# Optimization experiments

Hardware: AMD Instinct MI355X
Metric: run time of the kernel (lower is better)

Reference implementation:

```python
import jax, jax.numpy as jnp
import numpy as np

N_NODES = 24576
N_EDGES = 294912
B_GRAPHS = 128
D_IN = 92
D = 512
H = 8
HD = D // H
L = 3
DFF = 4 * D
LN_EPS = 1e-5


def _layer_norm(x, g, b):
    mu = jnp.mean(x, axis=-1, keepdims=True)
    var = jnp.mean((x - mu) ** 2, axis=-1, keepdims=True)
    return (x - mu) * jax.lax.rsqrt(var + LN_EPS) * g + b


def setup_inputs() -> dict:
    key = jax.random.key(0)
    ks = jax.random.split(key, 24)
    s = 0.02
    inp = {
        "node_features": jax.random.normal(ks[0], (N_NODES, D_IN), jnp.float32),
        "edge_index": jax.random.randint(ks[1], (2, N_EDGES), 0, N_NODES, jnp.int64),
        "edge_attr": jax.random.uniform(ks[2], (N_EDGES,), jnp.float32),
        "batch": jnp.sort(jax.random.randint(ks[3], (N_NODES,), 0, B_GRAPHS, jnp.int64)),
        # atom embedding Linear(92 -> D)
        "emb_w": jax.random.normal(ks[4], (D, D_IN), jnp.float32) * s,
        "emb_b": jnp.zeros((D,), jnp.float32),
        # per-layer MHA params (stacked over L layers)
        "in_proj_w": jax.random.normal(ks[5], (L, 3 * D, D), jnp.float32) * s,
        "in_proj_b": jnp.zeros((L, 3 * D), jnp.float32),
        "out_w": jax.random.normal(ks[6], (L, D, D), jnp.float32) * s,
        "out_b": jnp.zeros((L, D), jnp.float32),
        "ln1_g": jnp.ones((L, D), jnp.float32),
        "ln1_b": jnp.zeros((L, D), jnp.float32),
        "ffn_w1": jax.random.normal(ks[7], (L, DFF, D), jnp.float32) * s,
        "ffn_b1": jnp.zeros((L, DFF), jnp.float32),
        "ffn_w2": jax.random.normal(ks[8], (L, D, DFF), jnp.float32) * s,
        "ffn_b2": jnp.zeros((L, D), jnp.float32),
        "ln2_g": jnp.ones((L, D), jnp.float32),
        "ln2_b": jnp.zeros((L, D), jnp.float32),
        # output head: Linear(D,D) -> SiLU -> Linear(D,1)
        "head_w1": jax.random.normal(ks[9], (D, D), jnp.float32) * s,
        "head_b1": jnp.zeros((D,), jnp.float32),
        "head_w2": jax.random.normal(ks[10], (1, D), jnp.float32) * s,
        "head_b2": jnp.zeros((1,), jnp.float32),
    }
    return inp


def _forward(node_features, batch, emb_w, emb_b, in_proj_w, in_proj_b, out_w,
             out_b, ln1_g, ln1_b, ffn_w1, ffn_b1, ffn_w2, ffn_b2, ln2_g,
             ln2_b, head_w1, head_b1, head_w2, head_b2):
    N = node_features.shape[0]
    B = int(jnp.max(batch)) + 1
    counts = jnp.bincount(batch, length=B)            # (B,) nodes per graph
    S = int(jnp.max(counts))                          # max_nodes
    starts = jnp.searchsorted(batch, jnp.arange(B))   # batch is sorted
    pos = jnp.arange(N) - starts[batch]               # slot within graph

    h = node_features @ emb_w.T + emb_b               # (N, D)
    # ragged -> dense pad  (B, S, D)
    hp = jnp.zeros((B, S, D), h.dtype).at[batch, pos].set(h)
    key_pad = jnp.arange(S)[None, :] >= counts[:, None]   # True = padding

    scale = 1.0 / jnp.sqrt(jnp.asarray(HD, hp.dtype))
    for l in range(L):
        qkv = hp @ in_proj_w[l].T + in_proj_b[l]      # (B, S, 3D)
        q, k, v = jnp.split(qkv, 3, axis=-1)
        q = q.reshape(B, S, H, HD).transpose(0, 2, 1, 3)
        k = k.reshape(B, S, H, HD).transpose(0, 2, 1, 3)
        v = v.reshape(B, S, H, HD).transpose(0, 2, 1, 3)
        scores = jnp.einsum('bhqd,bhkd->bhqk', q, k) * scale
        scores = jnp.where(key_pad[:, None, None, :], -jnp.inf, scores)
        attn = jax.nn.softmax(scores, axis=-1)
        o = jnp.einsum('bhqk,bhkd->bhqd', attn, v)
        o = o.transpose(0, 2, 1, 3).reshape(B, S, D)
        o = o @ out_w[l].T + out_b[l]
        x = _layer_norm(hp + o, ln1_g[l], ln1_b[l])   # post-norm
        f = jax.nn.relu(x @ ffn_w1[l].T + ffn_b1[l]) @ ffn_w2[l].T + ffn_b2[l]
        hp = _layer_norm(x + f, ln2_g[l], ln2_b[l])

    # unpad + segment mean pool
    h_out = hp[batch, pos]                            # (N, D)
    pooled = jax.ops.segment_sum(h_out, batch, num_segments=B)
    pooled = pooled / counts[:, None].astype(pooled.dtype)
    y = jax.nn.silu(pooled @ head_w1.T + head_b1) @ head_w2.T + head_b2
    return y                                          # (B, 1)


def reference(node_features, edge_index, edge_attr, batch, emb_w, emb_b,
              in_proj_w, in_proj_b, out_w, out_b, ln1_g, ln1_b, ffn_w1,
              ffn_b1, ffn_w2, ffn_b2, ln2_g, ln2_b, head_w1, head_b1,
              head_w2, head_b2):
    # edge_index / edge_attr are accepted but unused, matching the torch forward
    return _forward(node_features, batch, emb_w, emb_b, in_proj_w, in_proj_b,
                    out_w, out_b, ln1_g, ln1_b, ffn_w1, ffn_b1, ffn_w2,
                    ffn_b2, ln2_g, ln2_b, head_w1, head_b1, head_w2, head_b2)
```

## Files before the change

kernel.cpp:

```cpp
#include <hip/hip_runtime.h>
#include <hip/hip_bf16.h>
#include <cstdint>
#include <cfloat>
#include <cstddef>
#include <type_traits>

#define N_NODES 24576
#define B_GRAPHS 128
#define D_IN 92
#define D_INP 96
#define DMODEL 512
#define NHEAD 8
#define HDIM 64
#define NLAYER 3
#define DFF 2048

typedef __attribute__((ext_vector_type(8))) short short8;
typedef __attribute__((ext_vector_type(4))) short short4v;
typedef __attribute__((ext_vector_type(8))) unsigned short ushort8;
typedef __attribute__((ext_vector_type(4))) float f32x4;

__device__ __forceinline__ float b2f(unsigned short u) {
  union { unsigned int i; float f; } x;
  x.i = ((unsigned int)u) << 16;
  return x.f;
}
__device__ __forceinline__ unsigned short f2b(float f) {
  __hip_bfloat16 h = __float2bfloat16(f);
  return *reinterpret_cast<unsigned short*>(&h);
}

__device__ __forceinline__ void gl2lds16(const __hip_bfloat16* g,
                                         __hip_bfloat16* l) {
  __builtin_amdgcn_global_load_lds(
      (const __attribute__((address_space(1))) unsigned int*)g,
      (__attribute__((address_space(3))) unsigned int*)l, 16, 0, 0);
}

__global__ void starts_k(const int* __restrict__ batch32, int* __restrict__ starts) {
  __shared__ int is64_s;
  const int tid = threadIdx.x;
  if (tid == 0) is64_s = 0;
  __syncthreads();
  int bad = 0;
  for (int i = tid; i < N_NODES - 1; i += 256)
    if (batch32[i] > batch32[i + 1]) bad = 1;
  if (bad) atomicOr(&is64_s, 1);
  __syncthreads();
  const int is64 = is64_s;
  if (tid <= B_GRAPHS) {
    int lo = 0, hi = N_NODES;
    while (lo < hi) {
      int mid = (lo + hi) >> 1;
      int v = is64 ? batch32[2 * mid] : batch32[mid];
      if (v < tid) lo = mid + 1; else hi = mid;
    }
    starts[tid] = lo;
  }
}

__global__ __launch_bounds__(256) void cvt_k(const float* __restrict__ in,
                                             __hip_bfloat16* __restrict__ out,
                                             int count4) {
  int i = blockIdx.x * 256 + threadIdx.x;
  if (i < count4) {
    float4 v = ((const float4*)in)[i];
    short4v o;
    o[0] = (short)f2b(v.x); o[1] = (short)f2b(v.y);
    o[2] = (short)f2b(v.z); o[3] = (short)f2b(v.w);
    ((short4v*)out)[i] = o;
  }
}

__global__ __launch_bounds__(256) void padcvt_k(const float* __restrict__ in,
                                                __hip_bfloat16* __restrict__ out,
                                                int rows) {
  int idx = blockIdx.x * 256 + threadIdx.x;
  if (idx < rows * D_INP) {
    int r = idx / D_INP, c = idx - r * D_INP;
    out[idx] = __float2bfloat16(c < D_IN ? in[(size_t)r * D_IN + c] : 0.0f);
  }
}

__global__ __launch_bounds__(256) void mgemm_k(
    const __hip_bfloat16* __restrict__ A, const __hip_bfloat16* __restrict__ W,
    const float* __restrict__ bias, const __hip_bfloat16* __restrict__ res,
    __hip_bfloat16* __restrict__ C, int M, int N, int K, int act) {
  __shared__ __align__(16) __hip_bfloat16 As[2][128 * 32];
  __shared__ __align__(16) __hip_bfloat16 Ws[2][128 * 32];
  const int tid = threadIdx.x;
  const int wave = tid >> 6, lane = tid & 63;

  const int nxt = N >> 7, nmt = M >> 7;
  int rowt, colt;
  if ((nmt & 7) == 0) {
    const int rows_per = nmt >> 3;
    const int x = blockIdx.x & 7;
    const int j = blockIdx.x >> 3;
    rowt = x * rows_per + j % rows_per;
    colt = j / rows_per;
  } else {
    rowt = blockIdx.x / nxt;
    colt = blockIdx.x % nxt;
  }
  const int m0 = rowt * 128, n0 = colt * 128;

  const int mw = (wave >> 1) * 64, nw = (wave & 1) * 64;
  const int quad = lane >> 4, l16 = lane & 15;

  f32x4 acc[4][4] = {};

  const int srow = wave * 32 + (lane >> 2);
  const int skc = (lane & 3) * 8;
  const __hip_bfloat16* gA = A + (size_t)(m0 + srow) * K + skc;
  const __hip_bfloat16* gW = W + (size_t)(n0 + srow) * K + skc;
  const int lo = wave * 32 * 32;

  gl2lds16(gA, &As[0][lo]);
  gl2lds16(gA + (size_t)16 * K, &As[0][lo + 16 * 32]);
  gl2lds16(gW, &Ws[0][lo]);
  gl2lds16(gW + (size_t)16 * K, &Ws[0][lo + 16 * 32]);

  int cur = 0;
  for (int k0 = 0; k0 < K; k0 += 32) {
    __syncthreads();
    if (k0 + 32 < K) {
      const int nb = cur ^ 1;
      gl2lds16(gA + k0 + 32, &As[nb][lo]);
      gl2lds16(gA + (size_t)16 * K + k0 + 32, &As[nb][lo + 16 * 32]);
      gl2lds16(gW + k0 + 32, &Ws[nb][lo]);
      gl2lds16(gW + (size_t)16 * K + k0 + 32, &Ws[nb][lo + 16 * 32]);
    }
    short8 af[4], bf[4];
#pragma unroll
    for (int t = 0; t < 4; t++) {
      af[t] = *(const short8*)&As[cur][(mw + t * 16 + l16) * 32 + quad * 8];
      bf[t] = *(const short8*)&Ws[cur][(nw + t * 16 + l16) * 32 + quad * 8];
    }
#pragma unroll
    for (int mt = 0; mt < 4; mt++)
#pragma unroll
      for (int nt = 0; nt < 4; nt++)
        acc[mt][nt] = __builtin_amdgcn_mfma_f32_16x16x32_bf16(
            af[mt], bf[nt], acc[mt][nt], 0, 0, 0);
    cur ^= 1;
  }

#pragma unroll
  for (int mt = 0; mt < 4; mt++) {
#pragma unroll
    for (int nt = 0; nt < 4; nt++) {
      const int n = n0 + nw + nt * 16 + l16;
      const float bv = bias[n];
#pragma unroll
      for (int i = 0; i < 4; i++) {
        const int m = m0 + mw + mt * 16 + quad * 4 + i;
        float v = acc[mt][nt][i] + bv;
        if (res) v += __bfloat162float(res[(size_t)m * N + n]);
        if (act == 1) v = fmaxf(v, 0.0f);
        C[(size_t)m * N + n] = __float2bfloat16(v);
      }
    }
  }
}

__global__ __launch_bounds__(256) void gemm_k(
    const float* __restrict__ A, const float* __restrict__ W,
    const float* __restrict__ bias, const float* __restrict__ res,
    float* __restrict__ C, int M, int N, int K, int act) {
  __shared__ float As[16][68];
  __shared__ float Ws[16][68];
  const int tid = threadIdx.x;
  const int tx = tid & 15, ty = tid >> 4;
  const int m0 = blockIdx.y * 64, n0 = blockIdx.x * 64;
  const int lr = tid >> 2;
  const int lk = (tid & 3) * 4;
  float acc[4][4] = {{0.f}};
  for (int k0 = 0; k0 < K; k0 += 16) {
#pragma unroll
    for (int i = 0; i < 4; i++) {
      int k = k0 + lk + i;
      As[lk + i][lr] = (k < K) ? A[(size_t)(m0 + lr) * K + k] : 0.0f;
      Ws[lk + i][lr] = (k < K) ? W[(size_t)(n0 + lr) * K + k] : 0.0f;
    }
    __syncthreads();
#pragma unroll
    for (int kk = 0; kk < 16; kk++) {
      float4 a4 = *(const float4*)&As[kk][ty * 4];
      float4 w4 = *(const float4*)&Ws[kk][tx * 4];
      float a[4] = {a4.x, a4.y, a4.z, a4.w};
      float w[4] = {w4.x, w4.y, w4.z, w4.w};
#pragma unroll
      for (int i = 0; i < 4; i++)
#pragma unroll
        for (int j = 0; j < 4; j++) acc[i][j] += a[i] * w[j];
    }
    __syncthreads();
  }
#pragma unroll
  for (int i = 0; i < 4; i++) {
    int m = m0 + ty * 4 + i;
#pragma unroll
    for (int j = 0; j < 4; j++) {
      int n = n0 + tx * 4 + j;
      float v = acc[i][j] + bias[n];
      if (res) v += res[(size_t)m * N + n];
      if (act == 1) v = fmaxf(v, 0.0f);
      else if (act == 2) v = v / (1.0f + __expf(-v));
      C[(size_t)m * N + n] = v;
    }
  }
}

__global__ __launch_bounds__(256) void lnb_k(
    const __hip_bfloat16* __restrict__ in, const float* __restrict__ g,
    const float* __restrict__ b, __hip_bfloat16* __restrict__ out) {
  int row = blockIdx.x * 4 + (threadIdx.x >> 6);
  int lane = threadIdx.x & 63;
  const unsigned short* rp =
      (const unsigned short*)in + (size_t)row * DMODEL + lane * 8;
  ushort8 sv = *(const ushort8*)rp;
  float v[8];
  float s = 0.f;
#pragma unroll
  for (int i = 0; i < 8; i++) { v[i] = b2f(sv[i]); s += v[i]; }
#pragma unroll
  for (int off = 32; off; off >>= 1) s += __shfl_xor(s, off);
  float mu = s * (1.0f / DMODEL);
  float vs = 0.f;
#pragma unroll
  for (int i = 0; i < 8; i++) { float d = v[i] - mu; vs += d * d; }
#pragma unroll
  for (int off = 32; off; off >>= 1) vs += __shfl_xor(vs, off);
  float rs = rsqrtf(vs * (1.0f / DMODEL) + 1e-5f);
  ushort8 o;
#pragma unroll
  for (int i = 0; i < 8; i++) {
    int c = lane * 8 + i;
    o[i] = f2b((v[i] - mu) * rs * g[c] + b[c]);
  }
  *(ushort8*)((unsigned short*)out + (size_t)row * DMODEL + lane * 8) = o;
}

#define MAXNH 128
__global__ __launch_bounds__(256, 3) void attn5_k(
    const __hip_bfloat16* __restrict__ qkv, const int* __restrict__ starts,
    __hip_bfloat16* __restrict__ O1, __hip_bfloat16* __restrict__ O2,
    float* __restrict__ ml) {
  const int half = blockIdx.x & 1;
  const int gh = blockIdx.x >> 1;
  const int g = gh >> 3, h = gh & 7;
  int s0 = starts[g], s1 = starts[g + 1];
  s0 = min(max(s0, 0), N_NODES);
  s1 = min(max(s1, s0), N_NODES);
  const int n = s1 - s0, start = s0;
  if (n == 0) return;
  const int tid = threadIdx.x, wave = tid >> 6, lane = tid & 63;
  const int quad = lane >> 4, l16 = lane & 15;
  unsigned short* Oh = (unsigned short*)(half ? O2 : O1);

  __shared__ __align__(16) unsigned short Ks[128][72];
  __shared__ __align__(16) unsigned short Vt[64][136];
  __shared__ __align__(16) unsigned short Ps[4][16][136];

  if (n <= 2 * MAXNH) {
    const int nh1 = (n + 1) >> 1;
    const int k0g = half * nh1;
    const int nh = half ? (n - nh1) : nh1;
    const int ktq = (n + 15) >> 4;

    if (nh == 0) {
      for (int mt = wave; mt < ktq; mt += 4) {
        const int q = mt * 16 + l16;
        if (q < n) {
          short4v z = {0, 0, 0, 0};
#pragma unroll
          for (int dt = 0; dt < 4; dt++)
            *(short4v*)(Oh + (size_t)(start + q) * DMODEL + h * HDIM +
                        dt * 16 + quad * 4) = z;
          if (quad == 0) {
            float2 mlv = {-FLT_MAX, 0.0f};
            *(float2*)(ml + ((size_t)(start + q) * NHEAD + h) * 4 + half * 2) = mlv;
          }
        }
      }
      return;
    }

    for (int idx = tid; idx < nh * 8; idx += 256) {
      int r = idx >> 3, c = (idx & 7) * 8;
      *(ushort8*)&Ks[r][c] = *(const ushort8*)((const unsigned short*)qkv +
                                               (size_t)(start + k0g + r) * 1536 +
                                               512 + h * HDIM + c);
    }
    for (int idx = tid; idx < 16 * 8; idx += 256) {
      int r = nh + (idx >> 3), c = (idx & 7) * 8;
      if (r < 128) {
        ushort8 z = {0, 0, 0, 0, 0, 0, 0, 0};
        *(ushort8*)&Ks[r][c] = z;
      }
    }
    const int vr = tid & 31, dc8 = tid >> 5;
    for (int r0 = 0; r0 < nh; r0 += 32) {
      int r = r0 + vr;
      if (r < nh) {
        ushort8 v = *(const ushort8*)((const unsigned short*)qkv +
                                      (size_t)(start + k0g + r) * 1536 + 1024 +
                                      h * HDIM + dc8 * 8);
#pragma unroll
        for (int j = 0; j < 8; j++) Vt[dc8 * 8 + j][r] = v[j];
      }
    }
    for (int idx = tid; idx < 64 * 32; idx += 256) {
      int d = idx >> 5, r = nh + (idx & 31);
      if (r < 136) Vt[d][r] = 0;
    }
    __syncthreads();

    const int ktmax2 = (nh + 15) >> 4;
    const int nkc2 = (nh + 31) >> 5;
    const float scale = 0.125f;

    for (int mt = wave; mt < ktq; mt += 4) {
      const int qrow = start + min(mt * 16 + l16, n - 1);
      const short8 qf0 = *(const short8*)((const unsigned short*)qkv +
                                          (size_t)qrow * 1536 + h * HDIM + quad * 8);
      const short8 qf1 = *(const short8*)((const unsigned short*)qkv +
                                          (size_t)qrow * 1536 + h * HDIM + 32 + quad * 8);
      f32x4 sacc[8];
#pragma unroll
      for (int kt = 0; kt < 8; kt++) {
        if (kt < ktmax2) {
          const int krow = kt * 16 + l16;
          const short8 kf0 = *(const short8*)&Ks[krow][quad * 8];
          const short8 kf1 = *(const short8*)&Ks[krow][32 + quad * 8];
          f32x4 a = {0.f, 0.f, 0.f, 0.f};
          a = __builtin_amdgcn_mfma_f32_16x16x32_bf16(kf0, qf0, a, 0, 0, 0);
          a = __builtin_amdgcn_mfma_f32_16x16x32_bf16(kf1, qf1, a, 0, 0, 0);
          sacc[kt] = a;
        }
      }
      float mx = -FLT_MAX;
#pragma unroll
      for (int kt = 0; kt < 8; kt++) {
        if (kt < ktmax2) {
#pragma unroll
          for (int i = 0; i < 4; i++) {
            const int key = kt * 16 + quad * 4 + i;
            const float v = sacc[kt][i] * scale;
            sacc[kt][i] = v;
            if (key < nh) mx = fmaxf(mx, v);
          }
        }
      }
      mx = fmaxf(mx, __shfl_xor(mx, 16));
      mx = fmaxf(mx, __shfl_xor(mx, 32));
      float ls = 0.f;
#pragma unroll
      for (int kt = 0; kt < 8; kt++) {
        if (kt < ktmax2) {
#pragma unroll
          for (int i = 0; i < 4; i++) {
            const int key = kt * 16 + quad * 4 + i;
            const float p = (key < nh) ? __expf(sacc[kt][i] - mx) : 0.0f;
            sacc[kt][i] = p;
            ls += p;
          }
        }
      }
      ls += __shfl_xor(ls, 16);
      ls += __shfl_xor(ls, 32);
#pragma unroll
      for (int kt = 0; kt < 8; kt++) {
        if (kt < 2 * nkc2) {
          short4v pp;
#pragma unroll
          for (int i = 0; i < 4; i++) {
            const float p = (kt < ktmax2) ? sacc[kt][i] : 0.0f;
            pp[i] = (short)f2b(p);
          }
          *(short4v*)&Ps[wave][l16][kt * 16 + quad * 4] = pp;
        }
      }
      __threadfence_block();
      const int qv = mt * 16 + l16;
#pragma unroll
      for (int dt = 0; dt < 4; dt++) {
        f32x4 oa = {0.f, 0.f, 0.f, 0.f};
#pragma unroll
        for (int kc = 0; kc < 4; kc++) {
          if (kc < nkc2) {
            const short8 vf = *(const short8*)&Vt[dt * 16 + l16][kc * 32 + quad * 8];
            const short8 pf = *(const short8*)&Ps[wave][l16][kc * 32 + quad * 8];
            oa = __builtin_amdgcn_mfma_f32_16x16x32_bf16(vf, pf, oa, 0, 0, 0);
          }
        }
        if (qv < n) {
          short4v ov;
#pragma unroll
          for (int i = 0; i < 4; i++) ov[i] = (short)f2b(oa[i]);
          *(short4v*)(Oh + (size_t)(start + qv) * DMODEL + h * HDIM +
                      dt * 16 + quad * 4) = ov;
        }
      }
      if (qv < n && quad == 0) {
        float2 mlv = {mx, ls};
        *(float2*)(ml + ((size_t)(start + qv) * NHEAD + h) * 4 + half * 2) = mlv;
      }
    }
  } else {
    const float scale = 0.125f;
    int nn = min(n, 512);
    if (half == 1) {
      for (int qi = wave; qi < nn; qi += 4) {
        Oh[(size_t)(start + qi) * DMODEL + h * HDIM + lane] = 0;
        if (lane == 0) {
          float2 mlv = {-FLT_MAX, 0.0f};
          *(float2*)(ml + ((size_t)(start + qi) * NHEAD + h) * 4 + 2) = mlv;
        }
      }
      return;
    }
    for (int qi = wave; qi < nn; qi += 4) {
      float qd = __bfloat162float(
          qkv[(size_t)(start + qi) * (3 * DMODEL) + h * HDIM + lane]);
      float sreg[8];
#pragma unroll
      for (int t = 0; t < 8; t++) {
        float sc = -FLT_MAX;
        if (t * 64 < nn) {
          int k = t * 64 + lane, kc = min(k, nn - 1);
          const __hip_bfloat16* Kr =
              qkv + (size_t)(start + kc) * (3 * DMODEL) + DMODEL + h * HDIM;
          float a = 0.f;
#pragma unroll
          for (int d = 0; d < 64; d++)
            a += __shfl(qd, d) * __bfloat162float(Kr[d]);
          if (k < nn) sc = a * scale;
        }
        sreg[t] = sc;
      }
      float m = -FLT_MAX;
#pragma unroll
      for (int t = 0; t < 8; t++) m = fmaxf(m, sreg[t]);
#pragma unroll
      for (int off = 32; off; off >>= 1) m = fmaxf(m, __shfl_xor(m, off));
      float lsum = 0.f;
#pragma unroll
      for (int t = 0; t < 8; t++) {
        float p = (sreg[t] == -FLT_MAX) ? 0.0f : __expf(sreg[t] - m);
        sreg[t] = p;
        lsum += p;
      }
#pragma unroll
      for (int off = 32; off; off >>= 1) lsum += __shfl_xor(lsum, off);
      float inv_l = 1.0f / lsum;
      float o = 0.f;
#pragma unroll
      for (int t = 0; t < 8; t++) {
        int kb = t * 64;
        if (kb < nn) {
          int kmax = min(64, nn - kb);
          const __hip_bfloat16* Vb = qkv + (size_t)(start + kb) * (3 * DMODEL) +
                                     2 * DMODEL + h * HDIM + lane;
          for (int j = 0; j < kmax; j++)
            o += __shfl(sreg[t], j) *
                 __bfloat162float(Vb[(size_t)j * (3 * DMODEL)]);
        }
      }
      Oh[(size_t)(start + qi) * DMODEL + h * HDIM + lane] = f2b(o * inv_l);
      if (lane == 0) {
        float2 mlv = {0.0f, 1.0f};
        *(float2*)(ml + ((size_t)(start + qi) * NHEAD + h) * 4) = mlv;
      }
    }
  }
}

__global__ __launch_bounds__(256) void merge_k(
    const __hip_bfloat16* __restrict__ O1, const __hip_bfloat16* __restrict__ O2,
    const float* __restrict__ ml, __hip_bfloat16* __restrict__ out) {
  int t = blockIdx.x * 256 + threadIdx.x;
  int node = t >> 6;
  int rem = t & 63;
  int h = rem >> 3;
  int c8 = (rem & 7) * 8;
  float4 m4 = *(const float4*)(ml + ((size_t)node * NHEAD + h) * 4);
  float mm = fmaxf(m4.x, m4.z);
  float w1 = __expf(m4.x - mm), w2 = __expf(m4.z - mm);
  float inv = 1.0f / (w1 * m4.y + w2 * m4.w);
  size_t off = (size_t)node * DMODEL + h * HDIM + c8;
  ushort8 a = *(const ushort8*)((const unsigned short*)O1 + off);
  ushort8 b = *(const ushort8*)((const unsigned short*)O2 + off);
  ushort8 o;
#pragma unroll
  for (int i = 0; i < 8; i++)
    o[i] = f2b((w1 * b2f(a[i]) + w2 * b2f(b[i])) * inv);
  *(ushort8*)((unsigned short*)out + off) = o;
}

__global__ __launch_bounds__(256) void pool_k(
    const __hip_bfloat16* __restrict__ hp, const int* __restrict__ starts,
    float* __restrict__ pooled) {
  int g = blockIdx.x;
  int s0 = starts[g], s1 = starts[g + 1];
  s0 = min(max(s0, 0), N_NODES);
  s1 = min(max(s1, s0), N_NODES);
  int n = s1 - s0;
  float inv = n > 0 ? 1.0f / (float)n : 0.0f;
  int c = blockIdx.y * 256 + threadIdx.x;
  float acc = 0.f;
  for (int r = s0; r < s1; r++)
    acc += __bfloat162float(hp[(size_t)r * DMODEL + c]);
  pooled[(size_t)g * DMODEL + c] = acc * inv;
}

__global__ __launch_bounds__(256) void head2_k(
    const float* __restrict__ h1, const float* __restrict__ w2,
    const float* __restrict__ b2, float* __restrict__ y) {
  int row = blockIdx.x * 4 + (threadIdx.x >> 6);
  int lane = threadIdx.x & 63;
  float s = 0.f;
#pragma unroll
  for (int i = 0; i < 8; i++) {
    int c = lane + i * 64;
    s += h1[(size_t)row * DMODEL + c] * w2[c];
  }
#pragma unroll
  for (int off = 32; off; off >>= 1) s += __shfl_xor(s, off);
  if (lane == 0) y[row] = s + b2[0];
}

extern "C" void kernel_launch(void* const* d_in, const int* in_sizes, int n_in,
                              void* d_out, int out_size, void* d_ws,
                              size_t ws_size, hipStream_t stream) {
  const float* node_features = (const float*)d_in[0];
  const int* batch = (const int*)d_in[3];
  const float* emb_w = (const float*)d_in[4];
  const float* emb_b = (const float*)d_in[5];
  const float* in_proj_w = (const float*)d_in[6];
  const float* in_proj_b = (const float*)d_in[7];
  const float* out_w = (const float*)d_in[8];
  const float* out_b = (const float*)d_in[9];
  const float* ln1_g = (const float*)d_in[10];
  const float* ln1_b = (const float*)d_in[11];
  const float* ffn_w1 = (const float*)d_in[12];
  const float* ffn_b1 = (const float*)d_in[13];
  const float* ffn_w2 = (const float*)d_in[14];
  const float* ffn_b2 = (const float*)d_in[15];
  const float* ln2_g = (const float*)d_in[16];
  const float* ln2_b = (const float*)d_in[17];
  const float* head_w1 = (const float*)d_in[18];
  const float* head_b1 = (const float*)d_in[19];
  const float* head_w2 = (const float*)d_in[20];
  const float* head_b2 = (const float*)d_in[21];
  float* y = (float*)d_out;

  typedef __hip_bfloat16 bf;
  char* wsb = (char*)d_ws;
  int* starts = (int*)wsb;
  bf* nf_b = (bf*)(wsb + 1024);
  bf* wq_b = nf_b + (size_t)N_NODES * D_INP;
  bf* wo_b = wq_b + (size_t)NLAYER * 3 * DMODEL * DMODEL;
  bf* w1_b = wo_b + (size_t)NLAYER * DMODEL * DMODEL;
  bf* w2_b = w1_b + (size_t)NLAYER * DFF * DMODEL;
  bf* we_b = w2_b + (size_t)NLAYER * DMODEL * DFF;
  bf* hp   = we_b + (size_t)DMODEL * D_INP;
  bf* xb   = hp + (size_t)N_NODES * DMODEL;
  bf* t1b  = xb + (size_t)N_NODES * DMODEL;
  bf* qkvb = t1b + (size_t)N_NODES * DMODEL;
  float* pooled = (float*)(qkvb + (size_t)N_NODES * 3 * DMODEL);
  float* h1 = pooled + (size_t)B_GRAPHS * DMODEL;
  float* ml = h1 + (size_t)B_GRAPHS * DMODEL;

  starts_k<<<1, 256, 0, stream>>>(batch, starts);

  {
    int c4;
    c4 = NLAYER * 3 * DMODEL * DMODEL / 4;
    cvt_k<<<(c4 + 255) / 256, 256, 0, stream>>>(in_proj_w, wq_b, c4);
    c4 = NLAYER * DMODEL * DMODEL / 4;
    cvt_k<<<(c4 + 255) / 256, 256, 0, stream>>>(out_w, wo_b, c4);
    c4 = NLAYER * DFF * DMODEL / 4;
    cvt_k<<<(c4 + 255) / 256, 256, 0, stream>>>(ffn_w1, w1_b, c4);
    cvt_k<<<(c4 + 255) / 256, 256, 0, stream>>>(ffn_w2, w2_b, c4);
    padcvt_k<<<(N_NODES * D_INP + 255) / 256, 256, 0, stream>>>(node_features,
                                                                nf_b, N_NODES);
    padcvt_k<<<(DMODEL * D_INP + 255) / 256, 256, 0, stream>>>(emb_w, we_b,
                                                               DMODEL);
  }

  mgemm_k<<<(N_NODES / 128) * (DMODEL / 128), 256, 0, stream>>>(
      nf_b, we_b, emb_b, nullptr, hp, N_NODES, DMODEL, D_INP, 0);

  for (int l = 0; l < NLAYER; l++) {
    const bf* wq = wq_b + (size_t)l * 3 * DMODEL * DMODEL;
    const bf* wo = wo_b + (size_t)l * DMODEL * DMODEL;
    const bf* w1 = w1_b + (size_t)l * DFF * DMODEL;
    const bf* w2 = w2_b + (size_t)l * DMODEL * DFF;
    const float* ipb = in_proj_b + (size_t)l * 3 * DMODEL;
    const float* ob = out_b + (size_t)l * DMODEL;
    const float* b1 = ffn_b1 + (size_t)l * DFF;
    const float* b2 = ffn_b2 + (size_t)l * DMODEL;

    mgemm_k<<<(N_NODES / 128) * (3 * DMODEL / 128), 256, 0, stream>>>(
        hp, wq, ipb, nullptr, qkvb, N_NODES, 3 * DMODEL, DMODEL, 0);

    attn5_k<<<B_GRAPHS * NHEAD * 2, 256, 0, stream>>>(qkvb, starts, t1b, xb, ml);
    merge_k<<<N_NODES * 64 / 256, 256, 0, stream>>>(t1b, xb, ml, t1b);

    mgemm_k<<<(N_NODES / 128) * (DMODEL / 128), 256, 0, stream>>>(
        t1b, wo, ob, hp, xb, N_NODES, DMODEL, DMODEL, 0);
    lnb_k<<<N_NODES / 4, 256, 0, stream>>>(xb, ln1_g + l * DMODEL,
                                           ln1_b + l * DMODEL, xb);

    const int CHUNK = 18432;
    for (int r0 = 0; r0 < N_NODES; r0 += CHUNK) {
      int rows = min(N_NODES - r0, CHUNK);
      bf* ffh = qkvb;
      mgemm_k<<<(rows / 128) * (DFF / 128), 256, 0, stream>>>(
          xb + (size_t)r0 * DMODEL, w1, b1, nullptr, ffh, rows, DFF, DMODEL, 1);
      mgemm_k<<<(rows / 128) * (DMODEL / 128), 256, 0, stream>>>(
          ffh, w2, b2, xb + (size_t)r0 * DMODEL, t1b + (size_t)r0 * DMODEL,
          rows, DMODEL, DFF, 0);
    }
    lnb_k<<<N_NODES / 4, 256, 0, stream>>>(t1b, ln2_g + l * DMODEL,
                                           ln2_b + l * DMODEL, hp);
  }

  pool_k<<<dim3(B_GRAPHS, 2), 256, 0, stream>>>(hp, starts, pooled);
  gemm_k<<<dim3(DMODEL / 64, B_GRAPHS / 64), 256, 0, stream>>>(
      pooled, head_w1, head_b1, nullptr, h1, B_GRAPHS, DMODEL, DMODEL, 2);
  head2_k<<<B_GRAPHS / 4, 256, 0, stream>>>(h1, head_w2, head_b2, y);
}
```

Before: 1.391 ms.

## Triple-buffer GEMM LDS tiles and swizzle K-chunks to avoid bank conflicts

The bf16 MFMA GEMM moves from double to triple buffering of LDS tiles. Loads are now issued two iterations ahead, and a partial s_waitcnt vmcnt plus s_barrier replaces the full __syncthreads, so global-to-LDS copies overlap more with compute. The 8-element K chunk each row lands in is XOR-rotated by row index on store and un-rotated on read, aiming to cut LDS bank conflicts on the fragment reads. LDS use grows from 32KB to 48KB per block, which may lower occupancy. The hand-written waitcnt also relies on a specific count of outstanding vector memory ops.

```diff
diff --git a/kernel.cpp b/kernel.cpp
--- a/kernel.cpp
+++ b/kernel.cpp
@@ -86,8 +86,8 @@
     const __hip_bfloat16* __restrict__ A, const __hip_bfloat16* __restrict__ W,
     const float* __restrict__ bias, const __hip_bfloat16* __restrict__ res,
     __hip_bfloat16* __restrict__ C, int M, int N, int K, int act) {
-  __shared__ __align__(16) __hip_bfloat16 As[2][128 * 32];
-  __shared__ __align__(16) __hip_bfloat16 Ws[2][128 * 32];
+  __shared__ __align__(16) __hip_bfloat16 As[3][128 * 32];
+  __shared__ __align__(16) __hip_bfloat16 Ws[3][128 * 32];
   const int tid = threadIdx.x;
   const int wave = tid >> 6, lane = tid & 63;
 
@@ -111,31 +111,44 @@
   f32x4 acc[4][4] = {};
 
   const int srow = wave * 32 + (lane >> 2);
-  const int skc = (lane & 3) * 8;
+  const int skc = (((lane & 3) + ((lane >> 2) >> 1)) & 3) * 8;
   const __hip_bfloat16* gA = A + (size_t)(m0 + srow) * K + skc;
   const __hip_bfloat16* gW = W + (size_t)(n0 + srow) * K + skc;
   const int lo = wave * 32 * 32;
 
+  const int niter = K >> 5;
   gl2lds16(gA, &As[0][lo]);
   gl2lds16(gA + (size_t)16 * K, &As[0][lo + 16 * 32]);
   gl2lds16(gW, &Ws[0][lo]);
   gl2lds16(gW + (size_t)16 * K, &Ws[0][lo + 16 * 32]);
-
-  int cur = 0;
-  for (int k0 = 0; k0 < K; k0 += 32) {
-    __syncthreads();
-    if (k0 + 32 < K) {
-      const int nb = cur ^ 1;
-      gl2lds16(gA + k0 + 32, &As[nb][lo]);
-      gl2lds16(gA + (size_t)16 * K + k0 + 32, &As[nb][lo + 16 * 32]);
-      gl2lds16(gW + k0 + 32, &Ws[nb][lo]);
-      gl2lds16(gW + (size_t)16 * K + k0 + 32, &Ws[nb][lo + 16 * 32]);
-    }
+  if (niter > 1) {
+    gl2lds16(gA + 32, &As[1][lo]);
+    gl2lds16(gA + (size_t)16 * K + 32, &As[1][lo + 16 * 32]);
+    gl2lds16(gW + 32, &Ws[1][lo]);
+    gl2lds16(gW + (size_t)16 * K + 32, &Ws[1][lo + 16 * 32]);
+  }
+
+  const int prd = ((quad - (l16 >> 1)) & 3) * 8;
+
+  for (int it = 0; it < niter; ++it) {
+    if (it + 1 < niter)
+      asm volatile("s_waitcnt vmcnt(4)\n\ts_barrier" ::: "memory");
+    else
+      asm volatile("s_waitcnt vmcnt(0)\n\ts_barrier" ::: "memory");
+    if (it + 2 < niter) {
+      const int kpre = (it + 2) * 32;
+      const int nb = (it + 2) % 3;
+      gl2lds16(gA + kpre, &As[nb][lo]);
+      gl2lds16(gA + (size_t)16 * K + kpre, &As[nb][lo + 16 * 32]);
+      gl2lds16(gW + kpre, &Ws[nb][lo]);
+      gl2lds16(gW + (size_t)16 * K + kpre, &Ws[nb][lo + 16 * 32]);
+    }
+    const int cb = it % 3;
     short8 af[4], bf[4];
 #pragma unroll
     for (int t = 0; t < 4; t++) {
-      af[t] = *(const short8*)&As[cur][(mw + t * 16 + l16) * 32 + quad * 8];
-      bf[t] = *(const short8*)&Ws[cur][(nw + t * 16 + l16) * 32 + quad * 8];
+      af[t] = *(const short8*)&As[cb][(mw + t * 16 + l16) * 32 + prd];
+      bf[t] = *(const short8*)&Ws[cb][(nw + t * 16 + l16) * 32 + prd];
     }
 #pragma unroll
     for (int mt = 0; mt < 4; mt++)
@@ -143,7 +156,6 @@
       for (int nt = 0; nt < 4; nt++)
         acc[mt][nt] = __builtin_amdgcn_mfma_f32_16x16x32_bf16(
             af[mt], bf[nt], acc[mt][nt], 0, 0, 0);
-    cur ^= 1;
   }
 
 #pragma unroll
```

Measured after the change: 1.410 ms. No clear change (+1.3%).
